# Kernel optimization log

Hardware: AMD Instinct MI355X
Metric: run time of the kernel (lower is better)

## Reference

```python
import jax, jax.numpy as jnp
import numpy as np

N = 100000
E = 1600000
N_IN = 512
N_H = 128


def setup_inputs() -> dict:
    key = jax.random.key(0)
    ks = jax.random.split(key, 8)
    x = jax.random.normal(ks[0], (N, N_IN), dtype=jnp.float32)
    src = jax.random.randint(ks[1], (E,), 0, N, dtype=jnp.int32)
    dst = jax.random.randint(ks[2], (E,), 0, N, dtype=jnp.int32)
    perm = jax.random.permutation(ks[3], N).astype(jnp.int32)
    # GraphConv params (in_feats=512 -> out_feats=128), xavier-ish scale
    W = jax.random.normal(ks[4], (N_IN, N_H), dtype=jnp.float32) / np.sqrt(N_IN)
    b = jnp.zeros((N_H,), dtype=jnp.float32)
    alpha = jnp.full((N_H,), 0.25, dtype=jnp.float32)  # PReLU(n_h) init
    mlp_W = jax.random.normal(ks[5], (N_H, N_H), dtype=jnp.float32) / np.sqrt(N_H)
    mlp_b = jnp.zeros((N_H,), dtype=jnp.float32)
    return {"x": x, "src": src, "dst": dst, "perm": perm, "W": W, "b": b,
            "alpha": alpha, "mlp_W": mlp_W, "mlp_b": mlp_b, "batch_train": 0}


def _degree_norm(idx, n):
    deg = jax.ops.segment_sum(jnp.ones_like(idx, dtype=jnp.float32), idx, num_segments=n)
    return jnp.clip(deg, 1.0, None) ** -0.5  # [n]


def _gcn_layer(x, src, dst, W, b, alpha):
    n = x.shape[0]
    norm_out = _degree_norm(src, n)  # src-side out-degree norm
    norm_in = _degree_norm(dst, n)   # dst-side in-degree norm
    # in_feats > out_feats: apply weight first (DGL GraphConv ordering)
    h = x @ W                                  # [N, n_h]
    h = h * norm_out[:, None]
    agg = jax.ops.segment_sum(h[src], dst, num_segments=n)  # SpMM copy_u/sum
    agg = agg * norm_in[:, None] + b
    return jnp.where(agg >= 0, agg, alpha * agg)  # PReLU(n_h)


def reference(x, src, dst, perm, W, b, alpha, mlp_W, mlp_b, batch_train):
    z1 = _gcn_layer(x, src, dst, W, b, alpha)          # clean encoder
    z2 = _gcn_layer(x[perm], src, dst, W, b, alpha)    # corrupted encoder
    z1 = z1 @ mlp_W + mlp_b
    z2 = z2 @ mlp_W + mlp_b
    logit = jnp.concatenate((z1.sum(1), z2.sum(1)), axis=0)  # [2N]
    return logit
```

## Files before the change

### kernel.cpp

```cpp
#include <hip/hip_runtime.h>


typedef __bf16 bf16x8 __attribute__((ext_vector_type(8)));
typedef float f32x4 __attribute__((ext_vector_type(4)));

#define PAD 48
#define NBMAX 256
#define EPB 4096

__device__ inline unsigned short f2bf(float f) {
  unsigned u = __float_as_uint(f);
  u += 0x7fffu + ((u >> 16) & 1u);
  return (unsigned short)(u >> 16);
}
__device__ inline float2 bfpair(unsigned u) {
  float2 r;
  r.x = __uint_as_float(u << 16);
  r.y = __uint_as_float(u & 0xffff0000u);
  return r;
}

__device__ __forceinline__ void gld16(const void* g, void* l) {
  __builtin_amdgcn_global_load_lds(
      (const __attribute__((address_space(1))) void*)g,
      (__attribute__((address_space(3))) void*)l, 16, 0, 0);
}

__global__ __launch_bounds__(256) void k_bin(const int* __restrict__ src,
                                             const int* __restrict__ dst,
                                             int* __restrict__ gCntD,
                                             int* __restrict__ gCntS,
                                             int* __restrict__ dstbin,
                                             unsigned short* __restrict__ srcbin,
                                             int E, int NB, int CAP) {
  __shared__ int2 stage[EPB];
  __shared__ int cntD[NBMAX], cntS[NBMAX], baseD[NBMAX], baseS[NBMAX];
  const int tid = threadIdx.x;
  const int e0 = blockIdx.x * EPB;
  const int nloc = min(EPB, E - e0);

  for (int b = tid; b < NB; b += 256) { cntD[b] = 0; cntS[b] = 0; }
  __syncthreads();

#pragma unroll
  for (int it = 0; it < EPB / 256; ++it) {
    int i = it * 256 + tid;
    if (i < nloc) {
      int s = src[e0 + i];
      int d = dst[e0 + i];
      stage[i] = make_int2(s, d);
      atomicAdd(&cntD[d >> 9], 1);
      atomicAdd(&cntS[s >> 9], 1);
    }
  }
  __syncthreads();

  for (int b = tid; b < NB; b += 256) {
    baseD[b] = atomicAdd(&gCntD[b], cntD[b]);
    baseS[b] = atomicAdd(&gCntS[b], cntS[b]);
    cntD[b] = 0;
    cntS[b] = 0;
  }
  __syncthreads();

#pragma unroll
  for (int it = 0; it < EPB / 256; ++it) {
    int i = it * 256 + tid;
    if (i < nloc) {
      int2 sd = stage[i];
      int s = sd.x, d = sd.y;
      int bd = d >> 9;
      int p = atomicAdd(&cntD[bd], 1) + baseD[bd];
      if (p < CAP) dstbin[(size_t)bd * CAP + p] = (s << 9) | (d & 511);
      int bs = s >> 9;
      int q = atomicAdd(&cntS[bs], 1) + baseS[bs];
      if (q < CAP) srcbin[(size_t)bs * CAP + q] = (unsigned short)(s & 511);
    }
  }
}

__global__ __launch_bounds__(256) void k_csr(const int* __restrict__ gCntD,
                                             const int* __restrict__ dstbin,
                                             int* __restrict__ col,
                                             int* __restrict__ deg_d,
                                             float* __restrict__ norm_i,
                                             int N, int CAP) {
  __shared__ int cnt[512];
  const int b = blockIdx.x;
  const int tid = threadIdx.x;
  cnt[tid] = 0;
  cnt[tid + 256] = 0;
  __syncthreads();
  int cb = gCntD[b];
  if (cb > CAP) cb = CAP;
  const int* bin = dstbin + (size_t)b * CAP;
  for (int i = tid; i < cb; i += 256) {
    int rec = bin[i];
    int d9 = rec & 511;
    int s = rec >> 9;
    int pos = atomicAdd(&cnt[d9], 1);
    if (pos < PAD) col[((size_t)b * 512 + d9) * PAD + pos] = s;
  }
  __syncthreads();
  for (int t = tid; t < 512; t += 256) {
    int i = b * 512 + t;
    if (i < N) {
      int c = cnt[t];
      deg_d[i] = (c > PAD) ? PAD : c;
      norm_i[i] = rsqrtf((float)((c < 1) ? 1 : c));
    }
  }
}

__global__ __launch_bounds__(256) void k_shist(const int* __restrict__ gCntS,
                                               const unsigned short* __restrict__ srcbin,
                                               const int* __restrict__ perm,
                                               float* __restrict__ norm_o,
                                               int* __restrict__ inv,
                                               int N, int CAP) {
  __shared__ int hist[512];
  const int b = blockIdx.x;
  const int tid = threadIdx.x;
  hist[tid] = 0;
  hist[tid + 256] = 0;
  __syncthreads();
  int cb = gCntS[b];
  if (cb > CAP) cb = CAP;
  const unsigned short* bin = srcbin + (size_t)b * CAP;
  for (int i = tid; i < cb; i += 256) {
    atomicAdd(&hist[bin[i]], 1);
  }
  __syncthreads();
  for (int t = tid; t < 512; t += 256) {
    int i = b * 512 + t;
    if (i < N) {
      int h = hist[t];
      norm_o[i] = rsqrtf((float)((h < 1) ? 1 : h));
      inv[perm[i]] = i;
    }
  }
}

__global__ __launch_bounds__(256) void k_fill_dev(const int* __restrict__ src,
                                                  const int* __restrict__ dst,
                                                  int* __restrict__ deg_s,
                                                  int* __restrict__ cnt,
                                                  int* __restrict__ col, int E) {
  int t = blockIdx.x * 256 + threadIdx.x;
  int e0 = t * 4;
  if (e0 >= E) return;
  int e1 = (e0 + 4 < E) ? e0 + 4 : E;
  for (int e = e0; e < e1; e++) {
    int s = src[e], d = dst[e];
    atomicAdd(&deg_s[s], 1);
    int pos = atomicAdd(&cnt[d], 1);
    if (pos < PAD) col[(size_t)d * PAD + pos] = s;
  }
}

__global__ __launch_bounds__(256) void k_finish_dev(const int* __restrict__ deg_s,
                                                    const int* __restrict__ cnt,
                                                    const int* __restrict__ perm,
                                                    float* __restrict__ norm_o,
                                                    float* __restrict__ norm_i,
                                                    int* __restrict__ deg_d,
                                                    int* __restrict__ inv, int N) {
  int i = blockIdx.x * 256 + threadIdx.x;
  if (i >= N) return;
  int a = deg_s[i]; if (a < 1) a = 1;
  int b = cnt[i];
  deg_d[i] = (b > PAD) ? PAD : b;
  if (b < 1) b = 1;
  norm_o[i] = rsqrtf((float)a);
  norm_i[i] = rsqrtf((float)b);
  inv[perm[i]] = i;
}

__global__ __launch_bounds__(256) void k_castw(const float* __restrict__ W,
                                               unsigned short* __restrict__ WT) {
  int i = blockIdx.x * 256 + threadIdx.x;
  int k = i >> 7;
  int n = i & 127;
  WT[n * 512 + k] = f2bf(W[i]);
}

__global__ __launch_bounds__(256) void k_gemm(const float* __restrict__ X,
                                              const unsigned short* __restrict__ WT,
                                              const float* __restrict__ norm_o,
                                              const int* __restrict__ inv,
                                              unsigned short* __restrict__ HH, int M) {
  __shared__ __align__(16) unsigned char lds_raw[32768];
  float* Asf = (float*)lds_raw;
  unsigned short* Bsh = (unsigned short*)(lds_raw + 16384);
  unsigned short* smem = (unsigned short*)lds_raw;

  const int tid = threadIdx.x;
  const int wave = tid >> 6;
  const int lane = tid & 63;
  const int m = lane & 15;
  const int quad = lane >> 4;
  const int block_row = blockIdx.x * 64;

  f32x4 acc[8];
#pragma unroll
  for (int t = 0; t < 8; t++) acc[t] = (f32x4){0.f, 0.f, 0.f, 0.f};

  const int ar0 = tid >> 3, as0 = (tid & 7) ^ (ar0 & 7);
  const int g1 = 256 + tid;
  const int ar1 = g1 >> 3, as1 = (g1 & 7) ^ (ar1 & 7);
  int gra0 = block_row + ar0; if (gra0 >= M) gra0 = M - 1;
  int gra1 = block_row + ar1; if (gra1 >= M) gra1 = M - 1;
  const float* srcA0 = X + (size_t)gra0 * 512 + as0 * 4;
  const float* srcA1 = X + (size_t)gra1 * 512 + as1 * 4;
  const int bn0 = tid >> 2, bs0 = (tid & 3) ^ ((bn0 >> 1) & 3);
  const int bn1 = g1 >> 2, bs1 = (g1 & 3) ^ ((bn1 >> 1) & 3);
  const unsigned short* srcB0 = WT + (size_t)bn0 * 512 + bs0 * 8;
  const unsigned short* srcB1 = WT + (size_t)bn1 * 512 + bs1 * 8;

  auto stage = [&](int buf, int kt) {
    const int k0 = kt * 32;
    float* la = Asf + buf * 2048;
    unsigned short* lb = Bsh + buf * 4096;
    gld16(srcA0 + k0, la + tid * 4);
    gld16(srcA1 + k0, la + g1 * 4);
    gld16(srcB0 + k0, lb + tid * 8);
    gld16(srcB1 + k0, lb + g1 * 8);
  };

  stage(0, 0);
  stage(1, 1);

  const int r = wave * 16 + m;
  const int sl0 = ((quad * 2) ^ (r & 7)) * 4;
  const int sl1 = ((quad * 2 + 1) ^ (r & 7)) * 4;

  int cur = 0;
#pragma unroll
  for (int kt = 0; kt < 16; ++kt) {
    if (kt < 15) {
      asm volatile("s_waitcnt vmcnt(4)" ::: "memory");
    } else {
      asm volatile("s_waitcnt vmcnt(0)" ::: "memory");
    }
    __builtin_amdgcn_s_barrier();
    __builtin_amdgcn_sched_barrier(0);
    const float* Ab = Asf + cur * 2048;
    const unsigned short* Bb = Bsh + cur * 4096;
    f32x4 a0 = *(const f32x4*)(Ab + r * 32 + sl0);
    f32x4 a1 = *(const f32x4*)(Ab + r * 32 + sl1);
    union { bf16x8 v; __bf16 h[8]; } au;
#pragma unroll
    for (int j = 0; j < 4; ++j) {
      au.h[j] = (__bf16)a0[j];
      au.h[4 + j] = (__bf16)a1[j];
    }
#pragma unroll
    for (int t = 0; t < 8; ++t) {
      int R = t * 16 + m;
      int bslot = quad ^ ((R >> 1) & 3);
      bf16x8 b = *(const bf16x8*)(Bb + R * 32 + bslot * 8);
      acc[t] = __builtin_amdgcn_mfma_f32_16x16x32_bf16(au.v, b, acc[t], 0, 0, 0);
    }
    __builtin_amdgcn_sched_barrier(0);
    __builtin_amdgcn_s_barrier();
    if (kt < 14) stage(cur, kt + 2);
    cur ^= 1;
  }

  float no1[4], no2[4];
#pragma unroll
  for (int rr4 = 0; rr4 < 4; rr4++) {
    int rr = block_row + wave * 16 + quad * 4 + rr4;
    no1[rr4] = 0.f;
    no2[rr4] = 0.f;
    if (rr < M) {
      no1[rr4] = norm_o[rr];
      no2[rr4] = norm_o[inv[rr]];
    }
  }

#pragma unroll
  for (int t = 0; t < 8; t++) {
    int c = t * 16 + m;
#pragma unroll
    for (int rr4 = 0; rr4 < 4; rr4++) {
      int row = wave * 16 + quad * 4 + rr4;
      smem[row * 128 + c] = f2bf(acc[t][rr4] * no1[rr4]);
    }
  }
  __syncthreads();
#pragma unroll
  for (int it = 0; it < 4; it++) {
    int idx = tid + it * 256;
    int row = idx >> 4;
    int c8 = (idx & 15) * 8;
    int gr = block_row + row;
    if (gr < M)
      *(int4*)(HH + (size_t)gr * 256 + c8) = *(int4*)&smem[row * 128 + c8];
  }
  __syncthreads();

#pragma unroll
  for (int t = 0; t < 8; t++) {
    int c = t * 16 + m;
#pragma unroll
    for (int rr4 = 0; rr4 < 4; rr4++) {
      int row = wave * 16 + quad * 4 + rr4;
      smem[row * 128 + c] = f2bf(acc[t][rr4] * no2[rr4]);
    }
  }
  __syncthreads();
#pragma unroll
  for (int it = 0; it < 4; it++) {
    int idx = tid + it * 256;
    int row = idx >> 4;
    int c8 = (idx & 15) * 8;
    int gr = block_row + row;
    if (gr < M) {
      int q = inv[gr];
      *(int4*)(HH + (size_t)q * 256 + 128 + c8) = *(int4*)&smem[row * 128 + c8];
    }
  }
}

__global__ __launch_bounds__(128) void k_wsum(const float* __restrict__ mlpW,
                                              const float* __restrict__ mlpb,
                                              float* __restrict__ wsum,
                                              float* __restrict__ bsum) {
  __shared__ float sb[128];
  int k = threadIdx.x;
  float s = 0.f;
  for (int j = 0; j < 128; j++) s += mlpW[k * 128 + j];
  wsum[k] = s;
  sb[k] = mlpb[k];
  __syncthreads();
  for (int off = 64; off > 0; off >>= 1) {
    if (k < off) sb[k] += sb[k + off];
    __syncthreads();
  }
  if (k == 0) bsum[0] = sb[0];
}

__global__ __launch_bounds__(256) void k_agg(const unsigned short* __restrict__ HH,
                                             const int* __restrict__ deg_d,
                                             const int* __restrict__ col,
                                             const float* __restrict__ norm_i,
                                             const float* __restrict__ bias,
                                             const float* __restrict__ alpha,
                                             const float* __restrict__ wsum,
                                             const float* __restrict__ bsum,
                                             float* __restrict__ out, int N) {
  int wave = (blockIdx.x * 256 + threadIdx.x) >> 6;
  int lane = threadIdx.x & 63;
  if (wave >= N) return;
  const int g = lane >> 4;
  const int sl = lane & 15;

  int cl = deg_d[wave];
  const int* cbase = col + (size_t)wave * PAD;

  float a1[8], a2[8];
#pragma unroll
  for (int i = 0; i < 8; i++) { a1[i] = 0.f; a2[i] = 0.f; }

  for (int j0 = 0; j0 < cl; j0 += 16) {
    int4 r1[4], r2[4];
    float mk[4];
#pragma unroll
    for (int u = 0; u < 4; ++u) {
      int j = j0 + u * 4 + g;
      int je = (j < cl) ? j : cl - 1;
      int s = cbase[je];
      mk[u] = (j < cl) ? 1.f : 0.f;
      const unsigned short* rp = HH + (size_t)s * 256 + sl * 8;
      r1[u] = *(const int4*)rp;
      r2[u] = *(const int4*)(rp + 128);
    }
#pragma unroll
    for (int u = 0; u < 4; ++u) {
      const unsigned* u1 = (const unsigned*)&r1[u];
      const unsigned* u2 = (const unsigned*)&r2[u];
#pragma unroll
      for (int q = 0; q < 4; q++) {
        float2 v1 = bfpair(u1[q]);
        float2 v2 = bfpair(u2[q]);
        a1[2 * q]     = fmaf(v1.x, mk[u], a1[2 * q]);
        a1[2 * q + 1] = fmaf(v1.y, mk[u], a1[2 * q + 1]);
        a2[2 * q]     = fmaf(v2.x, mk[u], a2[2 * q]);
        a2[2 * q + 1] = fmaf(v2.y, mk[u], a2[2 * q + 1]);
      }
    }
  }

#pragma unroll
  for (int i = 0; i < 8; i++) {
    a1[i] += __shfl_xor(a1[i], 16);
    a1[i] += __shfl_xor(a1[i], 32);
    a2[i] += __shfl_xor(a2[i], 16);
    a2[i] += __shfl_xor(a2[i], 32);
  }

  float ni = norm_i[wave];
  float4 bb0 = ((const float4*)bias)[sl * 2];
  float4 bb1 = ((const float4*)bias)[sl * 2 + 1];
  float4 al0 = ((const float4*)alpha)[sl * 2];
  float4 al1 = ((const float4*)alpha)[sl * 2 + 1];
  float4 ws0 = ((const float4*)wsum)[sl * 2];
  float4 ws1 = ((const float4*)wsum)[sl * 2 + 1];
  float bs = bsum[0];
  float bb[8] = {bb0.x, bb0.y, bb0.z, bb0.w, bb1.x, bb1.y, bb1.z, bb1.w};
  float al[8] = {al0.x, al0.y, al0.z, al0.w, al1.x, al1.y, al1.z, al1.w};
  float wsv[8] = {ws0.x, ws0.y, ws0.z, ws0.w, ws1.x, ws1.y, ws1.z, ws1.w};

  float p1 = 0.f, p2 = 0.f;
#pragma unroll
  for (int i = 0; i < 8; i++) {
    float g1 = a1[i] * ni + bb[i];
    float g2 = a2[i] * ni + bb[i];
    g1 = (g1 >= 0.f) ? g1 : al[i] * g1;
    g2 = (g2 >= 0.f) ? g2 : al[i] * g2;
    p1 = fmaf(g1, wsv[i], p1);
    p2 = fmaf(g2, wsv[i], p2);
  }
#pragma unroll
  for (int off = 8; off > 0; off >>= 1) {
    p1 += __shfl_down(p1, off);
    p2 += __shfl_down(p2, off);
  }
  if (lane == 0) {
    out[wave] = p1 + bs;
    out[N + wave] = p2 + bs;
  }
}


extern "C" void kernel_launch(void* const* d_in, const int* in_sizes, int n_in,
                              void* d_out, int out_size, void* d_ws, size_t ws_size,
                              hipStream_t stream) {
  const float* x = (const float*)d_in[0];
  const int* src = (const int*)d_in[1];
  const int* dst = (const int*)d_in[2];
  const int* perm = (const int*)d_in[3];
  const float* W = (const float*)d_in[4];
  const float* bias = (const float*)d_in[5];
  const float* alpha = (const float*)d_in[6];
  const float* mlpW = (const float*)d_in[7];
  const float* mlpb = (const float*)d_in[8];

  const int E = in_sizes[1];
  const int N = in_sizes[3];
  float* out = (float*)d_out;

  char* ws = (char*)d_ws;
  size_t off = 0;
  auto alloc = [&](size_t bytes) -> void* {
    void* p = ws + off;
    off = (off + bytes + 255) & ~(size_t)255;
    return p;
  };

  unsigned short* HH = (unsigned short*)alloc((size_t)N * 256 * sizeof(unsigned short));
  int* col = (int*)alloc((size_t)N * PAD * sizeof(int));
  unsigned short* WT = (unsigned short*)alloc(512 * 128 * sizeof(unsigned short));
  float* norm_o = (float*)alloc((size_t)N * sizeof(float));
  float* norm_i = (float*)alloc((size_t)N * sizeof(float));
  int* inv = (int*)alloc((size_t)N * sizeof(int));
  int* deg_d = (int*)alloc((size_t)N * sizeof(int));
  float* wsum = (float*)alloc(512);
  float* bsum = (float*)alloc(256);
  size_t common = off;

  const int NB = (N + 511) >> 9;
  const int meanB = (NB > 0) ? E / NB : 0;
  const int CAP = ((meanB * 5) / 4 + 1023) & ~1023;

  size_t need_binned = common + (size_t)NB * CAP * sizeof(int) +
                       (size_t)NB * CAP * sizeof(unsigned short) +
                       2 * (size_t)NBMAX * sizeof(int) + 4096;
  bool binned = (NB <= NBMAX) && ((ws_size == 0) || (ws_size >= need_binned));

  const int nbN = (N + 255) / 256;
  const int nbE4 = ((E + 3) / 4 + 255) / 256;

  k_castw<<<512 * 128 / 256, 256, 0, stream>>>(W, WT);
  k_wsum<<<1, 128, 0, stream>>>(mlpW, mlpb, wsum, bsum);

  if (binned) {
    int* dstbin = (int*)alloc((size_t)NB * CAP * sizeof(int));
    unsigned short* srcbin = (unsigned short*)alloc((size_t)NB * CAP * sizeof(unsigned short));
    int* gCntD = (int*)alloc((size_t)NBMAX * sizeof(int));
    int* gCntS = (int*)alloc((size_t)NBMAX * sizeof(int));
    hipMemsetAsync(gCntD, 0, (size_t)NBMAX * sizeof(int), stream);
    hipMemsetAsync(gCntS, 0, (size_t)NBMAX * sizeof(int), stream);
    const int nbBin = (E + EPB - 1) / EPB;
    k_bin<<<nbBin, 256, 0, stream>>>(src, dst, gCntD, gCntS, dstbin, srcbin,
                                     E, NB, CAP);
    k_csr<<<NB, 256, 0, stream>>>(gCntD, dstbin, col, deg_d, norm_i, N, CAP);
    k_shist<<<NB, 256, 0, stream>>>(gCntS, srcbin, perm, norm_o, inv, N, CAP);
  } else {
    int* deg_s = (int*)alloc((size_t)N * sizeof(int));
    int* cnt = (int*)alloc((size_t)N * sizeof(int));
    hipMemsetAsync(deg_s, 0, (size_t)N * sizeof(int), stream);
    hipMemsetAsync(cnt, 0, (size_t)N * sizeof(int), stream);
    k_fill_dev<<<nbE4, 256, 0, stream>>>(src, dst, deg_s, cnt, col, E);
    k_finish_dev<<<nbN, 256, 0, stream>>>(deg_s, cnt, perm, norm_o, norm_i,
                                          deg_d, inv, N);
  }

  k_gemm<<<(N + 63) / 64, 256, 0, stream>>>(x, WT, norm_o, inv, HH, N);
  k_agg<<<(N + 3) / 4, 256, 0, stream>>>(HH, deg_d, col, norm_i,
                                         bias, alpha, wsum, bsum, out, N);
}
```

Measured before the change: 511.7 us.

## Keep edges in registers for binning, merge CSR/hist kernels, load GEMM A directly

The binning kernel now keeps each thread's edges and their local slot offsets in registers, which removes the LDS staging array and the second round of shared atomics. The CSR build and the source histogram are merged into one kernel, saving a launch. The GEMM no longer stages A through LDS. Each lane reads its X row straight from global memory with a one-step register prefetch, while B is staged in 64-wide K chunks with double buffering. The risk is more register pressure and uncoalesced 32-byte-per-lane global reads of X in the GEMM.

```diff
diff --git a/kernel.cpp b/kernel.cpp
--- a/kernel.cpp
+++ b/kernel.cpp
@@ -7,6 +7,7 @@
 #define PAD 48
 #define NBMAX 256
 #define EPB 4096
+#define EPT 16
 
 __device__ inline unsigned short f2bf(float f) {
   unsigned u = __float_as_uint(f);
@@ -33,24 +34,25 @@
                                              int* __restrict__ dstbin,
                                              unsigned short* __restrict__ srcbin,
                                              int E, int NB, int CAP) {
-  __shared__ int2 stage[EPB];
   __shared__ int cntD[NBMAX], cntS[NBMAX], baseD[NBMAX], baseS[NBMAX];
   const int tid = threadIdx.x;
   const int e0 = blockIdx.x * EPB;
-  const int nloc = min(EPB, E - e0);
-
-  for (int b = tid; b < NB; b += 256) { cntD[b] = 0; cntS[b] = 0; }
-  __syncthreads();
-
-#pragma unroll
-  for (int it = 0; it < EPB / 256; ++it) {
-    int i = it * 256 + tid;
-    if (i < nloc) {
-      int s = src[e0 + i];
-      int d = dst[e0 + i];
-      stage[i] = make_int2(s, d);
-      atomicAdd(&cntD[d >> 9], 1);
-      atomicAdd(&cntS[s >> 9], 1);
+
+  for (int b = tid; b < NBMAX; b += 256) { cntD[b] = 0; cntS[b] = 0; }
+  __syncthreads();
+
+  int sv[EPT], dv[EPT], pd[EPT], ps[EPT];
+#pragma unroll
+  for (int it = 0; it < EPT; ++it) {
+    int e = e0 + it * 256 + tid;
+    sv[it] = -1;
+    if (e < E) {
+      int s = src[e];
+      int d = dst[e];
+      sv[it] = s;
+      dv[it] = d;
+      pd[it] = atomicAdd(&cntD[d >> 9], 1);
+      ps[it] = atomicAdd(&cntS[s >> 9], 1);
     }
   }
   __syncthreads();
@@ -58,82 +60,64 @@
   for (int b = tid; b < NB; b += 256) {
     baseD[b] = atomicAdd(&gCntD[b], cntD[b]);
     baseS[b] = atomicAdd(&gCntS[b], cntS[b]);
-    cntD[b] = 0;
-    cntS[b] = 0;
-  }
-  __syncthreads();
-
-#pragma unroll
-  for (int it = 0; it < EPB / 256; ++it) {
-    int i = it * 256 + tid;
-    if (i < nloc) {
-      int2 sd = stage[i];
-      int s = sd.x, d = sd.y;
+  }
+  __syncthreads();
+
+#pragma unroll
+  for (int it = 0; it < EPT; ++it) {
+    if (sv[it] >= 0) {
+      int s = sv[it], d = dv[it];
       int bd = d >> 9;
-      int p = atomicAdd(&cntD[bd], 1) + baseD[bd];
+      int p = baseD[bd] + pd[it];
       if (p < CAP) dstbin[(size_t)bd * CAP + p] = (s << 9) | (d & 511);
       int bs = s >> 9;
-      int q = atomicAdd(&cntS[bs], 1) + baseS[bs];
+      int q = baseS[bs] + ps[it];
       if (q < CAP) srcbin[(size_t)bs * CAP + q] = (unsigned short)(s & 511);
     }
   }
 }
 
-__global__ __launch_bounds__(256) void k_csr(const int* __restrict__ gCntD,
-                                             const int* __restrict__ dstbin,
-                                             int* __restrict__ col,
-                                             int* __restrict__ deg_d,
-                                             float* __restrict__ norm_i,
-                                             int N, int CAP) {
+__global__ __launch_bounds__(256) void k_post(const int* __restrict__ gCntD,
+                                              const int* __restrict__ dstbin,
+                                              const int* __restrict__ gCntS,
+                                              const unsigned short* __restrict__ srcbin,
+                                              const int* __restrict__ perm,
+                                              int* __restrict__ col,
+                                              int* __restrict__ deg_d,
+                                              float* __restrict__ norm_i,
+                                              float* __restrict__ norm_o,
+                                              int* __restrict__ inv,
+                                              int N, int CAP) {
   __shared__ int cnt[512];
+  __shared__ int hist[512];
   const int b = blockIdx.x;
   const int tid = threadIdx.x;
-  cnt[tid] = 0;
-  cnt[tid + 256] = 0;
-  __syncthreads();
-  int cb = gCntD[b];
-  if (cb > CAP) cb = CAP;
-  const int* bin = dstbin + (size_t)b * CAP;
-  for (int i = tid; i < cb; i += 256) {
-    int rec = bin[i];
+  cnt[tid] = 0; cnt[tid + 256] = 0;
+  hist[tid] = 0; hist[tid + 256] = 0;
+  __syncthreads();
+
+  int cbD = gCntD[b]; if (cbD > CAP) cbD = CAP;
+  const int* binD = dstbin + (size_t)b * CAP;
+  for (int i = tid; i < cbD; i += 256) {
+    int rec = binD[i];
     int d9 = rec & 511;
     int s = rec >> 9;
     int pos = atomicAdd(&cnt[d9], 1);
     if (pos < PAD) col[((size_t)b * 512 + d9) * PAD + pos] = s;
   }
-  __syncthreads();
+  int cbS = gCntS[b]; if (cbS > CAP) cbS = CAP;
+  const unsigned short* binS = srcbin + (size_t)b * CAP;
+  for (int i = tid; i < cbS; i += 256) {
+    atomicAdd(&hist[binS[i]], 1);
+  }
+  __syncthreads();
+
   for (int t = tid; t < 512; t += 256) {
     int i = b * 512 + t;
     if (i < N) {
       int c = cnt[t];
       deg_d[i] = (c > PAD) ? PAD : c;
       norm_i[i] = rsqrtf((float)((c < 1) ? 1 : c));
-    }
-  }
-}
-
-__global__ __launch_bounds__(256) void k_shist(const int* __restrict__ gCntS,
-                                               const unsigned short* __restrict__ srcbin,
-                                               const int* __restrict__ perm,
-                                               float* __restrict__ norm_o,
-                                               int* __restrict__ inv,
-                                               int N, int CAP) {
-  __shared__ int hist[512];
-  const int b = blockIdx.x;
-  const int tid = threadIdx.x;
-  hist[tid] = 0;
-  hist[tid + 256] = 0;
-  __syncthreads();
-  int cb = gCntS[b];
-  if (cb > CAP) cb = CAP;
-  const unsigned short* bin = srcbin + (size_t)b * CAP;
-  for (int i = tid; i < cb; i += 256) {
-    atomicAdd(&hist[bin[i]], 1);
-  }
-  __syncthreads();
-  for (int t = tid; t < 512; t += 256) {
-    int i = b * 512 + t;
-    if (i < N) {
       int h = hist[t];
       norm_o[i] = rsqrtf((float)((h < 1) ? 1 : h));
       inv[perm[i]] = i;
@@ -189,10 +173,8 @@
                                               const float* __restrict__ norm_o,
                                               const int* __restrict__ inv,
                                               unsigned short* __restrict__ HH, int M) {
-  __shared__ __align__(16) unsigned char lds_raw[32768];
-  float* Asf = (float*)lds_raw;
-  unsigned short* Bsh = (unsigned short*)(lds_raw + 16384);
-  unsigned short* smem = (unsigned short*)lds_raw;
+  __shared__ __align__(16) unsigned short Bs[2][128 * 64];
+  unsigned short* smem = &Bs[0][0];
 
   const int tid = threadIdx.x;
   const int wave = tid >> 6;
@@ -201,69 +183,67 @@
   const int quad = lane >> 4;
   const int block_row = blockIdx.x * 64;
 
+  int arow = block_row + wave * 16 + m;
+  if (arow >= M) arow = M - 1;
+  const float* xrow = X + (size_t)arow * 512 + quad * 8;
+
+  const unsigned short* srcB[4];
+  int dstB[4];
+#pragma unroll
+  for (int u = 0; u < 4; ++u) {
+    int L = tid + u * 256;
+    int n = L >> 3;
+    int s = L & 7;
+    int sp = s ^ (n & 7);
+    srcB[u] = WT + (size_t)n * 512 + sp * 8;
+    dstB[u] = n * 64 + s * 8;
+  }
+
   f32x4 acc[8];
 #pragma unroll
   for (int t = 0; t < 8; t++) acc[t] = (f32x4){0.f, 0.f, 0.f, 0.f};
 
-  const int ar0 = tid >> 3, as0 = (tid & 7) ^ (ar0 & 7);
-  const int g1 = 256 + tid;
-  const int ar1 = g1 >> 3, as1 = (g1 & 7) ^ (ar1 & 7);
-  int gra0 = block_row + ar0; if (gra0 >= M) gra0 = M - 1;
-  int gra1 = block_row + ar1; if (gra1 >= M) gra1 = M - 1;
-  const float* srcA0 = X + (size_t)gra0 * 512 + as0 * 4;
-  const float* srcA1 = X + (size_t)gra1 * 512 + as1 * 4;
-  const int bn0 = tid >> 2, bs0 = (tid & 3) ^ ((bn0 >> 1) & 3);
-  const int bn1 = g1 >> 2, bs1 = (g1 & 3) ^ ((bn1 >> 1) & 3);
-  const unsigned short* srcB0 = WT + (size_t)bn0 * 512 + bs0 * 8;
-  const unsigned short* srcB1 = WT + (size_t)bn1 * 512 + bs1 * 8;
-
-  auto stage = [&](int buf, int kt) {
-    const int k0 = kt * 32;
-    float* la = Asf + buf * 2048;
-    unsigned short* lb = Bsh + buf * 4096;
-    gld16(srcA0 + k0, la + tid * 4);
-    gld16(srcA1 + k0, la + g1 * 4);
-    gld16(srcB0 + k0, lb + tid * 8);
-    gld16(srcB1 + k0, lb + g1 * 8);
+  auto stageB = [&](int buf, int c) {
+    const int k0 = c * 64;
+#pragma unroll
+    for (int u = 0; u < 4; ++u) gld16(srcB[u] + k0, &Bs[buf][dstB[u]]);
   };
 
-  stage(0, 0);
-  stage(1, 1);
-
-  const int r = wave * 16 + m;
-  const int sl0 = ((quad * 2) ^ (r & 7)) * 4;
-  const int sl1 = ((quad * 2 + 1) ^ (r & 7)) * 4;
+  stageB(0, 0);
+  f32x4 a0 = *(const f32x4*)(xrow);
+  f32x4 a1 = *(const f32x4*)(xrow + 4);
+  __syncthreads();
 
   int cur = 0;
 #pragma unroll
-  for (int kt = 0; kt < 16; ++kt) {
-    if (kt < 15) {
-      asm volatile("s_waitcnt vmcnt(4)" ::: "memory");
-    } else {
-      asm volatile("s_waitcnt vmcnt(0)" ::: "memory");
-    }
-    __builtin_amdgcn_s_barrier();
-    __builtin_amdgcn_sched_barrier(0);
-    const float* Ab = Asf + cur * 2048;
-    const unsigned short* Bb = Bsh + cur * 4096;
-    f32x4 a0 = *(const f32x4*)(Ab + r * 32 + sl0);
-    f32x4 a1 = *(const f32x4*)(Ab + r * 32 + sl1);
-    union { bf16x8 v; __bf16 h[8]; } au;
-#pragma unroll
-    for (int j = 0; j < 4; ++j) {
-      au.h[j] = (__bf16)a0[j];
-      au.h[4 + j] = (__bf16)a1[j];
-    }
-#pragma unroll
-    for (int t = 0; t < 8; ++t) {
-      int R = t * 16 + m;
-      int bslot = quad ^ ((R >> 1) & 3);
-      bf16x8 b = *(const bf16x8*)(Bb + R * 32 + bslot * 8);
-      acc[t] = __builtin_amdgcn_mfma_f32_16x16x32_bf16(au.v, b, acc[t], 0, 0, 0);
-    }
-    __builtin_amdgcn_sched_barrier(0);
-    __builtin_amdgcn_s_barrier();
-    if (kt < 14) stage(cur, kt + 2);
+  for (int c = 0; c < 8; ++c) {
+    if (c < 7) stageB(cur ^ 1, c + 1);
+#pragma unroll
+    for (int st = 0; st < 2; ++st) {
+      const int ks = c * 2 + st;
+      f32x4 na0 = (f32x4){0.f, 0.f, 0.f, 0.f};
+      f32x4 na1 = (f32x4){0.f, 0.f, 0.f, 0.f};
+      if (ks < 15) {
+        na0 = *(const f32x4*)(xrow + (ks + 1) * 32);
+        na1 = *(const f32x4*)(xrow + (ks + 1) * 32 + 4);
+      }
+      union { bf16x8 v; __bf16 h[8]; } au;
+#pragma unroll
+      for (int j = 0; j < 4; ++j) {
+        au.h[j] = (__bf16)a0[j];
+        au.h[4 + j] = (__bf16)a1[j];
+      }
+      const int q = st * 4 + quad;
+#pragma unroll
+      for (int t = 0; t < 8; ++t) {
+        int R = t * 16 + m;
+        bf16x8 b = *(const bf16x8*)&Bs[cur][R * 64 + ((q ^ (R & 7)) * 8)];
+        acc[t] = __builtin_amdgcn_mfma_f32_16x16x32_bf16(au.v, b, acc[t], 0, 0, 0);
+      }
+      a0 = na0;
+      a1 = na1;
+    }
+    __syncthreads();
     cur ^= 1;
   }
 
@@ -495,8 +475,8 @@
     const int nbBin = (E + EPB - 1) / EPB;
     k_bin<<<nbBin, 256, 0, stream>>>(src, dst, gCntD, gCntS, dstbin, srcbin,
                                      E, NB, CAP);
-    k_csr<<<NB, 256, 0, stream>>>(gCntD, dstbin, col, deg_d, norm_i, N, CAP);
-    k_shist<<<NB, 256, 0, stream>>>(gCntS, srcbin, perm, norm_o, inv, N, CAP);
+    k_post<<<NB, 256, 0, stream>>>(gCntD, dstbin, gCntS, srcbin, perm, col,
+                                   deg_d, norm_i, norm_o, inv, N, CAP);
   } else {
     int* deg_s = (int*)alloc((size_t)N * sizeof(int));
     int* cnt = (int*)alloc((size_t)N * sizeof(int));
```

New measurement: 510.5 us. Within noise of the previous version (-0.2%).
